# Performance work log

Hardware: AMD Instinct MI355X
Metric: run time of the kernel (lower is better)

Reference implementation:

```python
import jax, jax.numpy as jnp
import numpy as np

N_FILTER = 32
NCENTS = 1024
BETA = 0.25  # commitment cost


def setup_inputs() -> dict:
    key = jax.random.key(0)
    k1, k2 = jax.random.split(key)
    lat = jax.random.normal(k1, (2048, 2048), dtype=jnp.float32)
    centroids = jax.random.normal(k2, (NCENTS, N_FILTER), dtype=jnp.float32)
    leak_factor = jnp.ones((), dtype=jnp.float32)
    return {"lat": lat, "centroids": centroids, "leak_factor": leak_factor}


def _vq(z, centroids):
    # z: [B, L, D]; centroids: [K, D]
    zf = z.reshape(-1, z.shape[-1])  # [N, D]
    # squared distances: ||z||^2 - 2 z.c + ||c||^2  -> [N, K]
    d = (jnp.sum(zf * zf, axis=1, keepdims=True)
         - 2.0 * zf @ centroids.T
         + jnp.sum(centroids * centroids, axis=1)[None, :])
    idx = jnp.argmin(d, axis=1)  # [N]
    zq = centroids[idx]  # gather, [N, D]
    sg = jax.lax.stop_gradient
    # VQ-VAE codebook + commitment losses
    loss = jnp.mean((sg(zf) - zq) ** 2) + BETA * jnp.mean((zf - sg(zq)) ** 2)
    # straight-through estimator
    zq_st = zf + sg(zq - zf)
    return zq_st.reshape(z.shape), loss


def reference(lat, centroids, leak_factor):
    B = lat.shape[0]
    lat_size = lat.shape[1]
    z = lat.reshape(B, lat_size // N_FILTER, N_FILTER)
    _zq, cent_loss = _vq(z, centroids)
    # NOTE: original forward overwrites the quantized result with raw lat
    new_lat = lat.reshape(B, lat_size)
    lf = jnp.clip(leak_factor, 0.001, 1000.0)
    return new_lat * lf, cent_loss
```

## Files before the change

### kernel.cpp

```cpp
#include <hip/hip_runtime.h>

#define D 32
#define K 1024
#define N_ROWS 131072
#define TOTAL_ELEMS 4194304
#define LOSS_SCALE (1.25f / 4194304.0f)
#define BIAS 192.0f

typedef __attribute__((ext_vector_type(8))) short short8;
typedef __attribute__((ext_vector_type(4))) float f32x4;

__device__ __forceinline__ unsigned short f2bf(float f) {
  unsigned u = __builtin_bit_cast(unsigned, f);
  unsigned r = u + 0x7FFFu + ((u >> 16) & 1u);
  return (unsigned short)(r >> 16);
}

__global__ __launch_bounds__(256) void prep_kernel(
    const float* __restrict__ cent, unsigned short* __restrict__ centbf,
    float* __restrict__ cnormb, float* __restrict__ loss_out) {
  int t = blockIdx.x * 256 + threadIdx.x;
  centbf[t] = f2bf(-2.0f * cent[t]);
  if (t == 0) *loss_out = 0.0f;
  if (t < K) {
    const float* c = cent + t * D;
    float s0 = 0.f, s1 = 0.f, s2 = 0.f, s3 = 0.f;
#pragma unroll
    for (int d = 0; d < D; d += 4) {
      s0 = fmaf(c[d], c[d], s0);
      s1 = fmaf(c[d + 1], c[d + 1], s1);
      s2 = fmaf(c[d + 2], c[d + 2], s2);
      s3 = fmaf(c[d + 3], c[d + 3], s3);
    }
    cnormb[t] = (s0 + s1) + (s2 + s3) + BIAS;
  }
}

__global__ __launch_bounds__(512) void vq_kernel(
    const float* __restrict__ lat, const float* __restrict__ cent,
    const unsigned short* __restrict__ centbf, const float* __restrict__ cnormb,
    const float* __restrict__ lf_ptr, float* __restrict__ out,
    float* __restrict__ loss_out) {
  __shared__ short8 sB8[4096];
  __shared__ float sCn[1024];
  __shared__ float wsum[8];
  const int tid = threadIdx.x;
  const int lane = tid & 63;
  const int wave = tid >> 6;
  const int quad = lane >> 4;
  const int col  = lane & 15;
  const int rowbase = blockIdx.x * 256 + wave * 32;

  {
    const short8* gB8 = (const short8*)centbf;
#pragma unroll
    for (int j = 0; j < 8; ++j) sB8[j * 512 + tid] = gB8[j * 512 + tid];
    sCn[tid] = cnormb[tid];
    sCn[512 + tid] = cnormb[512 + tid];
  }

  float lf = fminf(fmaxf(lf_ptr[0], 0.001f), 1000.0f);
  short8 a0, a1;
  {
    const float* p0 = lat + (size_t)(rowbase + col) * D + quad * 8;
    const float* p1 = p0 + 16 * D;
    float4 u0 = ((const float4*)p0)[0], u1 = ((const float4*)p0)[1];
    float4 w0 = ((const float4*)p1)[0], w1 = ((const float4*)p1)[1];
    a0[0] = (short)f2bf(u0.x); a0[1] = (short)f2bf(u0.y);
    a0[2] = (short)f2bf(u0.z); a0[3] = (short)f2bf(u0.w);
    a0[4] = (short)f2bf(u1.x); a0[5] = (short)f2bf(u1.y);
    a0[6] = (short)f2bf(u1.z); a0[7] = (short)f2bf(u1.w);
    a1[0] = (short)f2bf(w0.x); a1[1] = (short)f2bf(w0.y);
    a1[2] = (short)f2bf(w0.z); a1[3] = (short)f2bf(w0.w);
    a1[4] = (short)f2bf(w1.x); a1[5] = (short)f2bf(w1.y);
    a1[6] = (short)f2bf(w1.z); a1[7] = (short)f2bf(w1.w);
    float* o0 = out + (size_t)(rowbase + col) * D + quad * 8;
    float* o1 = o0 + 16 * D;
    float4 s00 = {u0.x * lf, u0.y * lf, u0.z * lf, u0.w * lf};
    float4 s01 = {u1.x * lf, u1.y * lf, u1.z * lf, u1.w * lf};
    float4 s10 = {w0.x * lf, w0.y * lf, w0.z * lf, w0.w * lf};
    float4 s11 = {w1.x * lf, w1.y * lf, w1.z * lf, w1.w * lf};
    ((float4*)o0)[0] = s00;
    ((float4*)o0)[1] = s01;
    ((float4*)o1)[0] = s10;
    ((float4*)o1)[1] = s11;
  }
  __syncthreads();

  const f32x4 zero = {0.f, 0.f, 0.f, 0.f};
  unsigned pk0[4] = {0xFFFFFFFFu, 0xFFFFFFFFu, 0xFFFFFFFFu, 0xFFFFFFFFu};
  unsigned pk1[4] = {0xFFFFFFFFu, 0xFFFFFFFFu, 0xFFFFFFFFu, 0xFFFFFFFFu};

  const int boff = col * 4 + quad;

  short8 b = sB8[boff];
  float cn = sCn[col];
  f32x4 d0 = __builtin_amdgcn_mfma_f32_16x16x32_bf16(a0, b, zero, 0, 0, 0);
  f32x4 d1 = __builtin_amdgcn_mfma_f32_16x16x32_bf16(a1, b, zero, 0, 0, 0);

#pragma unroll 7
  for (int f = 1; f < 64; ++f) {
    short8 bn = sB8[f * 64 + boff];
    float cnn = sCn[f * 16 + col];
    f32x4 e0 = __builtin_amdgcn_mfma_f32_16x16x32_bf16(a0, bn, zero, 0, 0, 0);
    f32x4 e1 = __builtin_amdgcn_mfma_f32_16x16x32_bf16(a1, bn, zero, 0, 0, 0);
    const unsigned idxv = (unsigned)(((f - 1) << 4) | col);
#pragma unroll
    for (int r = 0; r < 4; ++r) {
      float s0 = d0[r] + cn;
      unsigned q0 = (__builtin_bit_cast(unsigned, s0) & 0xFFFFFC00u) | idxv;
      pk0[r] = min(pk0[r], q0);
      float s1 = d1[r] + cn;
      unsigned q1 = (__builtin_bit_cast(unsigned, s1) & 0xFFFFFC00u) | idxv;
      pk1[r] = min(pk1[r], q1);
    }
    d0 = e0; d1 = e1; cn = cnn;
  }
  {
    const unsigned idxv = (unsigned)((63 << 4) | col);
#pragma unroll
    for (int r = 0; r < 4; ++r) {
      float s0 = d0[r] + cn;
      unsigned q0 = (__builtin_bit_cast(unsigned, s0) & 0xFFFFFC00u) | idxv;
      pk0[r] = min(pk0[r], q0);
      float s1 = d1[r] + cn;
      unsigned q1 = (__builtin_bit_cast(unsigned, s1) & 0xFFFFFC00u) | idxv;
      pk1[r] = min(pk1[r], q1);
    }
  }

#pragma unroll
  for (int off = 1; off < 16; off <<= 1) {
#pragma unroll
    for (int r = 0; r < 4; ++r) {
      unsigned o0 = __shfl_xor(pk0[r], off);
      pk0[r] = min(pk0[r], o0);
      unsigned o1 = __shfl_xor(pk1[r], off);
      pk1[r] = min(pk1[r], o1);
    }
  }

  const int rsel = lane & 3;
  const int q = (lane >> 2) & 3;
  float s = 0.f;
#pragma unroll
  for (int t = 0; t < 2; ++t) {
    unsigned pk = (t == 0) ? pk0[rsel] : pk1[rsel];
    int row = rowbase + t * 16 + quad * 4 + rsel;
    int ci = (int)(pk & 1023u);
    const float* zp = lat + (size_t)row * D + q * 8;
    const float* cp = cent + (size_t)ci * D + q * 8;
    float4 za = ((const float4*)zp)[0], zb = ((const float4*)zp)[1];
    float4 ca = ((const float4*)cp)[0], cb = ((const float4*)cp)[1];
    float f0 = za.x - ca.x, f1 = za.y - ca.y, f2 = za.z - ca.z, f3 = za.w - ca.w;
    float g0 = zb.x - cb.x, g1 = zb.y - cb.y, g2 = zb.z - cb.z, g3 = zb.w - cb.w;
    float m0 = fmaf(f0, f0, g0 * g0);
    float m1 = fmaf(f1, f1, g1 * g1);
    float m2 = fmaf(f2, f2, g2 * g2);
    float m3 = fmaf(f3, f3, g3 * g3);
    s += (m0 + m1) + (m2 + m3);
  }
  s += __shfl_xor(s, 4);
  s += __shfl_xor(s, 8);
  s += __shfl_xor(s, 1);
  s += __shfl_xor(s, 2);
  s += __shfl_xor(s, 16);
  s += __shfl_xor(s, 32);

  if (lane == 0) wsum[wave] = s;
  __syncthreads();
  if (tid == 0) {
    float blk = ((wsum[0] + wsum[1]) + (wsum[2] + wsum[3])) +
                ((wsum[4] + wsum[5]) + (wsum[6] + wsum[7]));
    atomicAdd(loss_out, blk * LOSS_SCALE);
  }
}

extern "C" void kernel_launch(void* const* d_in, const int* in_sizes, int n_in,
                              void* d_out, int out_size, void* d_ws, size_t ws_size,
                              hipStream_t stream) {
  const float* lat  = (const float*)d_in[0];
  const float* cent = (const float*)d_in[1];
  const float* lf   = (const float*)d_in[2];
  float* out = (float*)d_out;
  unsigned short* centbf = (unsigned short*)d_ws;
  float* cnormb = (float*)((char*)d_ws + K * D * sizeof(unsigned short));
  float* loss = out + TOTAL_ELEMS;

  prep_kernel<<<K * D / 256, 256, 0, stream>>>(cent, centbf, cnormb, loss);
  vq_kernel<<<N_ROWS / 256, 512, 0, stream>>>(lat, cent, centbf, cnormb, lf,
                                              out, loss);
}
```

Baseline: 96.60 us.

## Compute loss from min distance value instead of gathering argmin centroid

Replaces the packed argmin-index tracking and the follow-up gather of the chosen centroid with a plain float min over the biased distance. The loss is taken as ||z||^2 plus the minimum of (||c||^2 - 2 z.c), with ||z||^2 summed from the already-loaded row values. This removes the second global read of lat and the centroid gather, plus the bit-packing ALU work in the inner loop. The cost is that the loss now depends on bf16-rounded dot products instead of an exact fp32 recomputation, so it carries more numerical error, and the software-pipelined MFMA loop is simplified.

```diff
diff --git a/kernel.cpp b/kernel.cpp
--- a/kernel.cpp
+++ b/kernel.cpp
@@ -5,7 +5,6 @@
 #define N_ROWS 131072
 #define TOTAL_ELEMS 4194304
 #define LOSS_SCALE (1.25f / 4194304.0f)
-#define BIAS 192.0f
 
 typedef __attribute__((ext_vector_type(8))) short short8;
 typedef __attribute__((ext_vector_type(4))) float f32x4;
@@ -32,15 +31,14 @@
       s2 = fmaf(c[d + 2], c[d + 2], s2);
       s3 = fmaf(c[d + 3], c[d + 3], s3);
     }
-    cnormb[t] = (s0 + s1) + (s2 + s3) + BIAS;
+    cnormb[t] = (s0 + s1) + (s2 + s3);
   }
 }
 
 __global__ __launch_bounds__(512) void vq_kernel(
-    const float* __restrict__ lat, const float* __restrict__ cent,
-    const unsigned short* __restrict__ centbf, const float* __restrict__ cnormb,
-    const float* __restrict__ lf_ptr, float* __restrict__ out,
-    float* __restrict__ loss_out) {
+    const float* __restrict__ lat, const unsigned short* __restrict__ centbf,
+    const float* __restrict__ cnormb, const float* __restrict__ lf_ptr,
+    float* __restrict__ out, float* __restrict__ loss_out) {
   __shared__ short8 sB8[4096];
   __shared__ float sCn[1024];
   __shared__ float wsum[8];
@@ -61,6 +59,7 @@
 
   float lf = fminf(fmaxf(lf_ptr[0], 0.001f), 1000.0f);
   short8 a0, a1;
+  float zz;
   {
     const float* p0 = lat + (size_t)(rowbase + col) * D + quad * 8;
     const float* p1 = p0 + 16 * D;
@@ -74,6 +73,11 @@
     a1[2] = (short)f2bf(w0.z); a1[3] = (short)f2bf(w0.w);
     a1[4] = (short)f2bf(w1.x); a1[5] = (short)f2bf(w1.y);
     a1[6] = (short)f2bf(w1.z); a1[7] = (short)f2bf(w1.w);
+    float t0 = fmaf(u0.x, u0.x, fmaf(u0.y, u0.y, fmaf(u0.z, u0.z, u0.w * u0.w)));
+    float t1 = fmaf(u1.x, u1.x, fmaf(u1.y, u1.y, fmaf(u1.z, u1.z, u1.w * u1.w)));
+    float t2 = fmaf(w0.x, w0.x, fmaf(w0.y, w0.y, fmaf(w0.z, w0.z, w0.w * w0.w)));
+    float t3 = fmaf(w1.x, w1.x, fmaf(w1.y, w1.y, fmaf(w1.z, w1.z, w1.w * w1.w)));
+    zz = (t0 + t1) + (t2 + t3);
     float* o0 = out + (size_t)(rowbase + col) * D + quad * 8;
     float* o1 = o0 + 16 * D;
     float4 s00 = {u0.x * lf, u0.y * lf, u0.z * lf, u0.w * lf};
@@ -88,44 +92,21 @@
   __syncthreads();
 
   const f32x4 zero = {0.f, 0.f, 0.f, 0.f};
-  unsigned pk0[4] = {0xFFFFFFFFu, 0xFFFFFFFFu, 0xFFFFFFFFu, 0xFFFFFFFFu};
-  unsigned pk1[4] = {0xFFFFFFFFu, 0xFFFFFFFFu, 0xFFFFFFFFu, 0xFFFFFFFFu};
-
+  const float INF = 3.4e38f;
+  float m0[4] = {INF, INF, INF, INF};
+  float m1[4] = {INF, INF, INF, INF};
   const int boff = col * 4 + quad;
 
-  short8 b = sB8[boff];
-  float cn = sCn[col];
-  f32x4 d0 = __builtin_amdgcn_mfma_f32_16x16x32_bf16(a0, b, zero, 0, 0, 0);
-  f32x4 d1 = __builtin_amdgcn_mfma_f32_16x16x32_bf16(a1, b, zero, 0, 0, 0);
-
-#pragma unroll 7
-  for (int f = 1; f < 64; ++f) {
-    short8 bn = sB8[f * 64 + boff];
-    float cnn = sCn[f * 16 + col];
-    f32x4 e0 = __builtin_amdgcn_mfma_f32_16x16x32_bf16(a0, bn, zero, 0, 0, 0);
-    f32x4 e1 = __builtin_amdgcn_mfma_f32_16x16x32_bf16(a1, bn, zero, 0, 0, 0);
-    const unsigned idxv = (unsigned)(((f - 1) << 4) | col);
+#pragma unroll 8
+  for (int f = 0; f < 64; ++f) {
+    short8 b = sB8[f * 64 + boff];
+    float cn = sCn[f * 16 + col];
+    f32x4 d0 = __builtin_amdgcn_mfma_f32_16x16x32_bf16(a0, b, zero, 0, 0, 0);
+    f32x4 d1 = __builtin_amdgcn_mfma_f32_16x16x32_bf16(a1, b, zero, 0, 0, 0);
 #pragma unroll
     for (int r = 0; r < 4; ++r) {
-      float s0 = d0[r] + cn;
-      unsigned q0 = (__builtin_bit_cast(unsigned, s0) & 0xFFFFFC00u) | idxv;
-      pk0[r] = min(pk0[r], q0);
-      float s1 = d1[r] + cn;
-      unsigned q1 = (__builtin_bit_cast(unsigned, s1) & 0xFFFFFC00u) | idxv;
-      pk1[r] = min(pk1[r], q1);
-    }
-    d0 = e0; d1 = e1; cn = cnn;
-  }
-  {
-    const unsigned idxv = (unsigned)((63 << 4) | col);
-#pragma unroll
-    for (int r = 0; r < 4; ++r) {
-      float s0 = d0[r] + cn;
-      unsigned q0 = (__builtin_bit_cast(unsigned, s0) & 0xFFFFFC00u) | idxv;
-      pk0[r] = min(pk0[r], q0);
-      float s1 = d1[r] + cn;
-      unsigned q1 = (__builtin_bit_cast(unsigned, s1) & 0xFFFFFC00u) | idxv;
-      pk1[r] = min(pk1[r], q1);
+      m0[r] = fminf(m0[r], d0[r] + cn);
+      m1[r] = fminf(m1[r], d1[r] + cn);
     }
   }
 
@@ -133,41 +114,24 @@
   for (int off = 1; off < 16; off <<= 1) {
 #pragma unroll
     for (int r = 0; r < 4; ++r) {
-      unsigned o0 = __shfl_xor(pk0[r], off);
-      pk0[r] = min(pk0[r], o0);
-      unsigned o1 = __shfl_xor(pk1[r], off);
-      pk1[r] = min(pk1[r], o1);
+      m0[r] = fminf(m0[r], __shfl_xor(m0[r], off));
+      m1[r] = fminf(m1[r], __shfl_xor(m1[r], off));
     }
   }
 
-  const int rsel = lane & 3;
-  const int q = (lane >> 2) & 3;
-  float s = 0.f;
-#pragma unroll
-  for (int t = 0; t < 2; ++t) {
-    unsigned pk = (t == 0) ? pk0[rsel] : pk1[rsel];
-    int row = rowbase + t * 16 + quad * 4 + rsel;
-    int ci = (int)(pk & 1023u);
-    const float* zp = lat + (size_t)row * D + q * 8;
-    const float* cp = cent + (size_t)ci * D + q * 8;
-    float4 za = ((const float4*)zp)[0], zb = ((const float4*)zp)[1];
-    float4 ca = ((const float4*)cp)[0], cb = ((const float4*)cp)[1];
-    float f0 = za.x - ca.x, f1 = za.y - ca.y, f2 = za.z - ca.z, f3 = za.w - ca.w;
-    float g0 = zb.x - cb.x, g1 = zb.y - cb.y, g2 = zb.z - cb.z, g3 = zb.w - cb.w;
-    float m0 = fmaf(f0, f0, g0 * g0);
-    float m1 = fmaf(f1, f1, g1 * g1);
-    float m2 = fmaf(f2, f2, g2 * g2);
-    float m3 = fmaf(f3, f3, g3 * g3);
-    s += (m0 + m1) + (m2 + m3);
-  }
-  s += __shfl_xor(s, 4);
-  s += __shfl_xor(s, 8);
-  s += __shfl_xor(s, 1);
-  s += __shfl_xor(s, 2);
+  float s = ((m0[0] + m0[1]) + (m0[2] + m0[3])) +
+            ((m1[0] + m1[1]) + (m1[2] + m1[3]));
   s += __shfl_xor(s, 16);
   s += __shfl_xor(s, 32);
 
-  if (lane == 0) wsum[wave] = s;
+  zz += __shfl_xor(zz, 1);
+  zz += __shfl_xor(zz, 2);
+  zz += __shfl_xor(zz, 4);
+  zz += __shfl_xor(zz, 8);
+  zz += __shfl_xor(zz, 16);
+  zz += __shfl_xor(zz, 32);
+
+  if (lane == 0) wsum[wave] = s + zz;
   __syncthreads();
   if (tid == 0) {
     float blk = ((wsum[0] + wsum[1]) + (wsum[2] + wsum[3])) +
@@ -188,6 +152,6 @@
   float* loss = out + TOTAL_ELEMS;
 
   prep_kernel<<<K * D / 256, 256, 0, stream>>>(cent, centbf, cnormb, loss);
-  vq_kernel<<<N_ROWS / 256, 512, 0, stream>>>(lat, cent, centbf, cnormb, lf,
+  vq_kernel<<<N_ROWS / 256, 512, 0, stream>>>(lat, centbf, cnormb, lf,
                                               out, loss);
 }
```

Result: faster. 87.78 us (-9.1%).
